# Kernel tuning notes

Measured on AMD Instinct MI355X. Metric: run time of the kernel, lower is better.

The kernel has to match this reference:

```python
import jax, jax.numpy as jnp
import numpy as np

V = 50257   # vocab / ouput_size
H = 1024    # hidden_size
L = 4096    # encoder length
NL = 2      # num_layers


def setup_inputs() -> dict:
    key = jax.random.key(0)
    ks = jax.random.split(key, 20)
    s = 0.02
    f32 = jnp.float32
    return {
        "input": jax.random.randint(ks[0], (1, 1), 0, V),
        "hidden_state": jax.random.normal(ks[1], (NL, 1, H), f32),
        "enc_outputs": jax.random.normal(ks[2], (L, H), f32),
        # parameters
        "emb": jax.random.normal(ks[3], (V, H), f32) * s,
        "Wq": jax.random.normal(ks[4], (H, H), f32) * s,
        "Wk": jax.random.normal(ks[5], (H, H), f32) * s,
        "wv": jax.random.normal(ks[6], (H, 1), f32) * s,
        "W_ih0": jax.random.normal(ks[7], (3 * H, 2 * H), f32) * s,
        "W_hh0": jax.random.normal(ks[8], (3 * H, H), f32) * s,
        "b_ih0": jnp.zeros((3 * H,), f32),
        "b_hh0": jnp.zeros((3 * H,), f32),
        "W_ih1": jax.random.normal(ks[9], (3 * H, H), f32) * s,
        "W_hh1": jax.random.normal(ks[10], (3 * H, H), f32) * s,
        "b_ih1": jnp.zeros((3 * H,), f32),
        "b_hh1": jnp.zeros((3 * H,), f32),
        "Wd": jax.random.normal(ks[11], (H, V), f32) * s,
        "bd": jnp.zeros((V,), f32),
    }


def _gru_step(x, h, W_ih, W_hh, b_ih, b_hh):
    # PyTorch GRU cell: gates ordered (reset, update, new)
    gi = W_ih @ x + b_ih          # [3H]
    gh = W_hh @ h + b_hh          # [3H]
    i_r, i_z, i_n = jnp.split(gi, 3)
    h_r, h_z, h_n = jnp.split(gh, 3)
    r = jax.nn.sigmoid(i_r + h_r)
    z = jax.nn.sigmoid(i_z + h_z)
    n = jnp.tanh(i_n + r * h_n)
    return (1.0 - z) * n + z * h


def reference(input, hidden_state, enc_outputs, emb, Wq, Wk, wv,
              W_ih0, W_hh0, b_ih0, b_hh0, W_ih1, W_hh1, b_ih1, b_hh1,
              Wd, bd):
    # embedding + (dropout p=0 is identity) + relu  -> [H]
    emb_vec = jax.nn.relu(emb[input[0, 0]])
    # additive attention: query = last-layer hidden [H], keys/values = enc [L,H]
    query = hidden_state[-1, 0]
    feat = jnp.tanh(query @ Wq + enc_outputs @ Wk)   # [L,H] (broadcast add)
    scores = feat @ wv                               # [L,1]
    attn = jax.nn.softmax(scores, axis=0)            # softmax over L
    context = jnp.sum(attn * enc_outputs, axis=0)    # [H]
    # single-step 2-layer GRU on concat(context, embedded) -> [2H]
    x = jnp.concatenate([context, emb_vec])
    h0n = _gru_step(x, hidden_state[0, 0], W_ih0, W_hh0, b_ih0, b_hh0)
    h1n = _gru_step(h0n, hidden_state[1, 0], W_ih1, W_hh1, b_ih1, b_hh1)
    # dense + log_softmax over vocab
    logits = h1n @ Wd + bd                           # [V]
    logp = jax.nn.log_softmax(logits)[None, :]       # [1,V]
    new_hidden = jnp.stack([h0n, h1n])[:, None, :]   # [NL,1,H]
    return logp, new_hidden
```

## Files before the change

### kernel.cpp

```cpp
#include <hip/hip_runtime.h>
#include <hip/hip_bf16.h>

#define H  1024
#define L  4096
#define V  50257
#define H3 3072

#define OFF_QW     0
#define OFF_SCORES 1024
#define OFF_X      (1024 + 4096)
#define OFF_GI0    (OFF_X + 2048)
#define OFF_GH0    (OFF_GI0 + 3072)
#define OFF_GI1    (OFF_GH0 + 3072)
#define OFF_GH1    (OFF_GI1 + 3072)
#define OFF_LOGITS (OFF_GH1 + 3072)
#define WS_FLOATS  (OFF_LOGITS + V)

__global__ __launch_bounds__(256) void k_embed(const int* __restrict__ tok,
                                               const float* __restrict__ emb,
                                               float* __restrict__ ws) {
    int j = blockIdx.x * 256 + threadIdx.x;
    int t = tok[0];
    float v = emb[(size_t)t * H + j];
    ws[OFF_X + H + j] = fmaxf(v, 0.f);
}

__global__ __launch_bounds__(256) void k_qw(const float* __restrict__ Wq,
                                            const float* __restrict__ hid,
                                            float* __restrict__ ws) {
    int j = blockIdx.x * 256 + threadIdx.x;
    const float* q = hid + H;
    int i0 = blockIdx.y * 64;
    float acc = 0.f;
#pragma unroll 8
    for (int i = i0; i < i0 + 64; ++i) acc += q[i] * Wq[i * H + j];
    atomicAdd(&ws[OFF_QW + j], acc);
}

__global__ __launch_bounds__(256) void k_gemm_scores(const float* __restrict__ enc,
                                                     const float* __restrict__ Wk,
                                                     const float* __restrict__ wv,
                                                     float* __restrict__ ws) {
    __shared__ float As[32][68];
    __shared__ float Bs[32][68];
    const int tid = threadIdx.x;
    const int tx = tid & 15, ty = tid >> 4;
    const int m0 = blockIdx.x * 64, n0 = blockIdx.y * 64;

    float acc[4][4] = {};

    for (int k0 = 0; k0 < H; k0 += 32) {
#pragma unroll
        for (int s = 0; s < 2; ++s) {
            int u  = tid + s * 256;
            int r  = u >> 3;
            int kq = u & 7;
            float4 a = *(const float4*)(enc + (m0 + r) * H + k0 + kq * 4);
            As[kq * 4 + 0][r] = a.x;
            As[kq * 4 + 1][r] = a.y;
            As[kq * 4 + 2][r] = a.z;
            As[kq * 4 + 3][r] = a.w;
        }
#pragma unroll
        for (int s = 0; s < 2; ++s) {
            int u  = tid + s * 256;
            int k  = u >> 4;
            int nq = u & 15;
            *(float4*)(&Bs[k][nq * 4]) = *(const float4*)(Wk + (k0 + k) * H + n0 + nq * 4);
        }
        __syncthreads();
#pragma unroll
        for (int k = 0; k < 32; ++k) {
            float4 a = *(const float4*)(&As[k][ty * 4]);
            float4 b = *(const float4*)(&Bs[k][tx * 4]);
            acc[0][0] += a.x * b.x; acc[0][1] += a.x * b.y; acc[0][2] += a.x * b.z; acc[0][3] += a.x * b.w;
            acc[1][0] += a.y * b.x; acc[1][1] += a.y * b.y; acc[1][2] += a.y * b.z; acc[1][3] += a.y * b.w;
            acc[2][0] += a.z * b.x; acc[2][1] += a.z * b.y; acc[2][2] += a.z * b.z; acc[2][3] += a.z * b.w;
            acc[3][0] += a.w * b.x; acc[3][1] += a.w * b.y; acc[3][2] += a.w * b.z; acc[3][3] += a.w * b.w;
        }
        __syncthreads();
    }

    float4 qw4 = *(const float4*)(&ws[OFF_QW + n0 + tx * 4]);
    float4 wv4 = *(const float4*)(wv + n0 + tx * 4);
#pragma unroll
    for (int i = 0; i < 4; ++i) {
        float s = tanhf(acc[i][0] + qw4.x) * wv4.x
                + tanhf(acc[i][1] + qw4.y) * wv4.y
                + tanhf(acc[i][2] + qw4.z) * wv4.z
                + tanhf(acc[i][3] + qw4.w) * wv4.w;
#pragma unroll
        for (int off = 1; off < 16; off <<= 1) s += __shfl_down(s, off, 16);
        if (tx == 0) atomicAdd(&ws[OFF_SCORES + m0 + ty * 4 + i], s);
    }
}

__global__ __launch_bounds__(1024) void k_softmax(float* __restrict__ ws) {
    __shared__ float red[16];
    const int tid = threadIdx.x;
    float* sc = ws + OFF_SCORES;

    float m = -1e30f;
    for (int l = tid; l < L; l += 1024) m = fmaxf(m, sc[l]);
#pragma unroll
    for (int off = 32; off; off >>= 1) m = fmaxf(m, __shfl_down(m, off));
    if ((tid & 63) == 0) red[tid >> 6] = m;
    __syncthreads();
    if (tid == 0) {
        float mm = red[0];
        for (int w = 1; w < 16; ++w) mm = fmaxf(mm, red[w]);
        red[0] = mm;
    }
    __syncthreads();
    m = red[0];
    __syncthreads();

    float ssum = 0.f;
    for (int l = tid; l < L; l += 1024) ssum += expf(sc[l] - m);
#pragma unroll
    for (int off = 32; off; off >>= 1) ssum += __shfl_down(ssum, off);
    if ((tid & 63) == 0) red[tid >> 6] = ssum;
    __syncthreads();
    if (tid == 0) {
        float t = 0.f;
        for (int w = 0; w < 16; ++w) t += red[w];
        red[0] = t;
    }
    __syncthreads();
    float inv = 1.f / red[0];

    for (int l = tid; l < L; l += 1024) sc[l] = expf(sc[l] - m) * inv;
}

__global__ __launch_bounds__(256) void k_context(const float* __restrict__ enc,
                                                 float* __restrict__ ws) {
    int h = blockIdx.x * 256 + threadIdx.x;
    const float* attn = ws + OFF_SCORES;
    int l0 = blockIdx.y * 128;
    float acc = 0.f;
#pragma unroll 4
    for (int l = l0; l < l0 + 128; ++l) acc += attn[l] * enc[l * H + h];
    atomicAdd(&ws[OFF_X + h], acc);
}

__global__ __launch_bounds__(256) void k_gates(const float* __restrict__ Wih,
                                               const float* __restrict__ Whh,
                                               const float* __restrict__ bih,
                                               const float* __restrict__ bhh,
                                               const float* __restrict__ x, int Cx,
                                               const float* __restrict__ h,
                                               float* __restrict__ gi,
                                               float* __restrict__ gh) {
    int b = blockIdx.x;
    bool isH = (b >= 768);
    int row  = (isH ? b - 768 : b) * 4 + (threadIdx.x >> 6);
    int lane = threadIdx.x & 63;
    const float* W    = isH ? Whh : Wih;
    const float* v    = isH ? h : x;
    const float* bias = isH ? bhh : bih;
    int C       = isH ? H : Cx;
    float* out  = isH ? gh : gi;

    const float4* Wr = (const float4*)(W + (size_t)row * C);
    const float4* v4 = (const float4*)v;
    float acc = 0.f;
    int n4 = C >> 2;
    for (int c = lane; c < n4; c += 64) {
        float4 w = Wr[c], xx = v4[c];
        acc += w.x * xx.x + w.y * xx.y + w.z * xx.z + w.w * xx.w;
    }
#pragma unroll
    for (int off = 32; off; off >>= 1) acc += __shfl_down(acc, off);
    if (lane == 0) out[row] = acc + bias[row];
}

__global__ __launch_bounds__(256) void k_combine(const float* __restrict__ gi,
                                                 const float* __restrict__ gh,
                                                 const float* __restrict__ h,
                                                 float* __restrict__ hout) {
    int j = blockIdx.x * 256 + threadIdx.x;
    float r = 1.f / (1.f + expf(-(gi[j] + gh[j])));
    float z = 1.f / (1.f + expf(-(gi[H + j] + gh[H + j])));
    float n = tanhf(gi[2 * H + j] + r * gh[2 * H + j]);
    hout[j] = (1.f - z) * n + z * h[j];
}

__global__ __launch_bounds__(256) void k_logits(const float* __restrict__ Wd,
                                                const float* __restrict__ bd,
                                                const float* __restrict__ h1,
                                                float* __restrict__ ws) {
    int v = blockIdx.x * 256 + threadIdx.x;
    if (v >= V) return;
    int k0 = blockIdx.y * 128;
    float acc = (blockIdx.y == 0) ? bd[v] : 0.f;
#pragma unroll 4
    for (int k = k0; k < k0 + 128; ++k) acc += h1[k] * Wd[(size_t)k * V + v];
    atomicAdd(&ws[OFF_LOGITS + v], acc);
}

__global__ __launch_bounds__(1024) void k_logsoftmax(const float* __restrict__ lg,
                                                     float* __restrict__ out) {
    __shared__ float red[16];
    const int tid = threadIdx.x;

    float m = -1e30f;
    for (int v = tid; v < V; v += 1024) m = fmaxf(m, lg[v]);
#pragma unroll
    for (int off = 32; off; off >>= 1) m = fmaxf(m, __shfl_down(m, off));
    if ((tid & 63) == 0) red[tid >> 6] = m;
    __syncthreads();
    if (tid == 0) {
        float mm = red[0];
        for (int w = 1; w < 16; ++w) mm = fmaxf(mm, red[w]);
        red[0] = mm;
    }
    __syncthreads();
    m = red[0];
    __syncthreads();

    float s = 0.f;
    for (int v = tid; v < V; v += 1024) s += expf(lg[v] - m);
#pragma unroll
    for (int off = 32; off; off >>= 1) s += __shfl_down(s, off);
    if ((tid & 63) == 0) red[tid >> 6] = s;
    __syncthreads();
    if (tid == 0) {
        float t = 0.f;
        for (int w = 0; w < 16; ++w) t += red[w];
        red[0] = t;
    }
    __syncthreads();
    float lse = m + logf(red[0]);

    for (int v = tid; v < V; v += 1024) out[v] = lg[v] - lse;
}

extern "C" void kernel_launch(void* const* d_in, const int* in_sizes, int n_in,
                              void* d_out, int out_size, void* d_ws, size_t ws_size,
                              hipStream_t stream) {
    const int*   tok  = (const int*)d_in[0];
    const float* hid  = (const float*)d_in[1];
    const float* enc  = (const float*)d_in[2];
    const float* emb  = (const float*)d_in[3];
    const float* Wq   = (const float*)d_in[4];
    const float* Wk   = (const float*)d_in[5];
    const float* wv   = (const float*)d_in[6];
    const float* Wih0 = (const float*)d_in[7];
    const float* Whh0 = (const float*)d_in[8];
    const float* bih0 = (const float*)d_in[9];
    const float* bhh0 = (const float*)d_in[10];
    const float* Wih1 = (const float*)d_in[11];
    const float* Whh1 = (const float*)d_in[12];
    const float* bih1 = (const float*)d_in[13];
    const float* bhh1 = (const float*)d_in[14];
    const float* Wd   = (const float*)d_in[15];
    const float* bd   = (const float*)d_in[16];
    float* out = (float*)d_out;
    float* ws  = (float*)d_ws;

    hipMemsetAsync(ws, 0, WS_FLOATS * sizeof(float), stream);

    k_embed<<<4, 256, 0, stream>>>(tok, emb, ws);
    k_qw<<<dim3(4, 16), 256, 0, stream>>>(Wq, hid, ws);
    k_gemm_scores<<<dim3(L / 64, H / 64), 256, 0, stream>>>(enc, Wk, wv, ws);
    k_softmax<<<1, 1024, 0, stream>>>(ws);
    k_context<<<dim3(4, 32), 256, 0, stream>>>(enc, ws);

    k_gates<<<1536, 256, 0, stream>>>(Wih0, Whh0, bih0, bhh0,
                                      ws + OFF_X, 2 * H, hid,
                                      ws + OFF_GI0, ws + OFF_GH0);
    k_combine<<<4, 256, 0, stream>>>(ws + OFF_GI0, ws + OFF_GH0, hid, out + V);

    k_gates<<<1536, 256, 0, stream>>>(Wih1, Whh1, bih1, bhh1,
                                      out + V, H, hid + H,
                                      ws + OFF_GI1, ws + OFF_GH1);
    k_combine<<<4, 256, 0, stream>>>(ws + OFF_GI1, ws + OFF_GH1, hid + H, out + V + H);

    k_logits<<<dim3((V + 255) / 256, 8), 256, 0, stream>>>(Wd, bd, out + V + H, ws);
    k_logsoftmax<<<1, 1024, 0, stream>>>(ws + OFF_LOGITS, out);
}
```

Measured before the change: 618.7 us.

## Use bf16 MFMA for attention scores GEMM and fuse softmax, GRU combine stages

Transposes Wk to bf16 in a combined prep kernel and computes the L×H attention-feature GEMM with 32x32x16 bf16 MFMA instructions instead of FP32 FMA tiling. The softmax is folded into the context kernel, and the GRU combine steps are folded into the next gates and logits kernels, which removes several launches. The cost is bf16 rounding of the encoder and Wk inputs, an extra transpose pass over Wk on every call, and redundant recomputation of the softmax statistics and GRU combine in every block.

```diff
diff --git a/kernel.cpp b/kernel.cpp
--- a/kernel.cpp
+++ b/kernel.cpp
@@ -4,143 +4,161 @@
 #define H  1024
 #define L  4096
 #define V  50257
-#define H3 3072
 
 #define OFF_QW     0
 #define OFF_SCORES 1024
-#define OFF_X      (1024 + 4096)
-#define OFF_GI0    (OFF_X + 2048)
-#define OFF_GH0    (OFF_GI0 + 3072)
-#define OFF_GI1    (OFF_GH0 + 3072)
-#define OFF_GH1    (OFF_GI1 + 3072)
-#define OFF_LOGITS (OFF_GH1 + 3072)
-#define WS_FLOATS  (OFF_LOGITS + V)
-
-__global__ __launch_bounds__(256) void k_embed(const int* __restrict__ tok,
-                                               const float* __restrict__ emb,
-                                               float* __restrict__ ws) {
-    int j = blockIdx.x * 256 + threadIdx.x;
-    int t = tok[0];
-    float v = emb[(size_t)t * H + j];
-    ws[OFF_X + H + j] = fmaxf(v, 0.f);
-}
-
-__global__ __launch_bounds__(256) void k_qw(const float* __restrict__ Wq,
-                                            const float* __restrict__ hid,
-                                            float* __restrict__ ws) {
-    int j = blockIdx.x * 256 + threadIdx.x;
-    const float* q = hid + H;
-    int i0 = blockIdx.y * 64;
-    float acc = 0.f;
+#define OFF_X      5120
+#define OFF_GI0    7168
+#define OFF_GH0    10240
+#define OFF_GI1    13312
+#define OFF_GH1    16384
+#define OFF_LOGITS 19456
+#define ZERO_FLOATS (OFF_LOGITS + V)
+#define OFF_WKT_BYTES 278880
+
+typedef __bf16 bf8   __attribute__((ext_vector_type(8)));
+typedef float  f32x16 __attribute__((ext_vector_type(16)));
+
+__device__ inline unsigned int pack_bf16x2(float lo, float hi) {
+    unsigned int ulo = __builtin_bit_cast(unsigned int, lo);
+    unsigned int uhi = __builtin_bit_cast(unsigned int, hi);
+    return ((uhi + 0x8000u) & 0xFFFF0000u) | ((ulo + 0x8000u) >> 16);
+}
+__device__ inline unsigned short cvt_bf16(float f) {
+    unsigned int u = __builtin_bit_cast(unsigned int, f);
+    return (unsigned short)((u + 0x8000u) >> 16);
+}
+
+__global__ __launch_bounds__(256) void k_prep(const int* __restrict__ tok,
+                                              const float* __restrict__ emb,
+                                              const float* __restrict__ hid,
+                                              const float* __restrict__ Wq,
+                                              const float* __restrict__ Wk,
+                                              float* __restrict__ ws,
+                                              unsigned short* __restrict__ wkT) {
+    __shared__ float tile[32][33];
+    const int b = blockIdx.x, t = threadIdx.x;
+    if (b < 4) {
+        int j = b * 256 + t;
+        float v = emb[(size_t)tok[0] * H + j];
+        ws[OFF_X + H + j] = fmaxf(v, 0.f);
+    } else if (b < 68) {
+        int bb = b - 4;
+        int j = (bb & 3) * 256 + t;
+        int i0 = (bb >> 2) * 64;
+        const float* q = hid + H;
+        float acc = 0.f;
 #pragma unroll 8
-    for (int i = i0; i < i0 + 64; ++i) acc += q[i] * Wq[i * H + j];
-    atomicAdd(&ws[OFF_QW + j], acc);
+        for (int i = i0; i < i0 + 64; ++i) acc += q[i] * Wq[i * H + j];
+        atomicAdd(&ws[OFF_QW + j], acc);
+    } else {
+        int tt = b - 68;
+        int tk = tt & 31, tn = tt >> 5;
+        int c = t & 31, r0 = t >> 5;
+#pragma unroll
+        for (int rr = 0; rr < 4; ++rr) {
+            int r = r0 + rr * 8;
+            tile[r][c] = Wk[(size_t)(tk * 32 + r) * H + tn * 32 + c];
+        }
+        __syncthreads();
+#pragma unroll
+        for (int rr = 0; rr < 4; ++rr) {
+            int rn = r0 + rr * 8;
+            wkT[(size_t)(tn * 32 + rn) * H + tk * 32 + c] = cvt_bf16(tile[c][rn]);
+        }
+    }
 }
 
 __global__ __launch_bounds__(256) void k_gemm_scores(const float* __restrict__ enc,
-                                                     const float* __restrict__ Wk,
+                                                     const unsigned short* __restrict__ wkT,
                                                      const float* __restrict__ wv,
                                                      float* __restrict__ ws) {
-    __shared__ float As[32][68];
-    __shared__ float Bs[32][68];
-    const int tid = threadIdx.x;
-    const int tx = tid & 15, ty = tid >> 4;
-    const int m0 = blockIdx.x * 64, n0 = blockIdx.y * 64;
-
-    float acc[4][4] = {};
+    __shared__ unsigned short As[64][40];
+    __shared__ unsigned short Bs[128][40];
+    const int t = threadIdx.x, lane = t & 63, w = t >> 6;
+    const int m0 = blockIdx.x * 64, n0 = blockIdx.y * 128;
+
+    f32x16 acc0 = {}, acc1 = {};
+
+    const int ar = t >> 2, akq = (t & 3) * 8;
+    const int bn = t >> 1, bkh = (t & 1) * 16;
+
+    const int r0 = (w & 1) * 32, c0 = (w >> 1) * 64;
+    const int mrow = r0 + (lane & 31);
+    const int nrow0 = c0 + (lane & 31), nrow1 = nrow0 + 32;
 
     for (int k0 = 0; k0 < H; k0 += 32) {
-#pragma unroll
-        for (int s = 0; s < 2; ++s) {
-            int u  = tid + s * 256;
-            int r  = u >> 3;
-            int kq = u & 7;
-            float4 a = *(const float4*)(enc + (m0 + r) * H + k0 + kq * 4);
-            As[kq * 4 + 0][r] = a.x;
-            As[kq * 4 + 1][r] = a.y;
-            As[kq * 4 + 2][r] = a.z;
-            As[kq * 4 + 3][r] = a.w;
-        }
-#pragma unroll
-        for (int s = 0; s < 2; ++s) {
-            int u  = tid + s * 256;
-            int k  = u >> 4;
-            int nq = u & 15;
-            *(float4*)(&Bs[k][nq * 4]) = *(const float4*)(Wk + (k0 + k) * H + n0 + nq * 4);
-        }
+        float4 fa = *(const float4*)(enc + (size_t)(m0 + ar) * H + k0 + akq);
+        float4 fb = *(const float4*)(enc + (size_t)(m0 + ar) * H + k0 + akq + 4);
+        uint4 wb0 = *(const uint4*)(wkT + (size_t)(n0 + bn) * H + k0 + bkh);
+        uint4 wb1 = *(const uint4*)(wkT + (size_t)(n0 + bn) * H + k0 + bkh + 8);
         __syncthreads();
-#pragma unroll
-        for (int k = 0; k < 32; ++k) {
-            float4 a = *(const float4*)(&As[k][ty * 4]);
-            float4 b = *(const float4*)(&Bs[k][tx * 4]);
-            acc[0][0] += a.x * b.x; acc[0][1] += a.x * b.y; acc[0][2] += a.x * b.z; acc[0][3] += a.x * b.w;
-            acc[1][0] += a.y * b.x; acc[1][1] += a.y * b.y; acc[1][2] += a.y * b.z; acc[1][3] += a.y * b.w;
-            acc[2][0] += a.z * b.x; acc[2][1] += a.z * b.y; acc[2][2] += a.z * b.z; acc[2][3] += a.z * b.w;
-            acc[3][0] += a.w * b.x; acc[3][1] += a.w * b.y; acc[3][2] += a.w * b.z; acc[3][3] += a.w * b.w;
-        }
+        uint4 pa;
+        pa.x = pack_bf16x2(fa.x, fa.y); pa.y = pack_bf16x2(fa.z, fa.w);
+        pa.z = pack_bf16x2(fb.x, fb.y); pa.w = pack_bf16x2(fb.z, fb.w);
+        *(uint4*)&As[ar][akq] = pa;
+        *(uint4*)&Bs[bn][bkh] = wb0;
+        *(uint4*)&Bs[bn][bkh + 8] = wb1;
         __syncthreads();
-    }
-
-    float4 qw4 = *(const float4*)(&ws[OFF_QW + n0 + tx * 4]);
-    float4 wv4 = *(const float4*)(wv + n0 + tx * 4);
-#pragma unroll
-    for (int i = 0; i < 4; ++i) {
-        float s = tanhf(acc[i][0] + qw4.x) * wv4.x
-                + tanhf(acc[i][1] + qw4.y) * wv4.y
-                + tanhf(acc[i][2] + qw4.z) * wv4.z
-                + tanhf(acc[i][3] + qw4.w) * wv4.w;
-#pragma unroll
-        for (int off = 1; off < 16; off <<= 1) s += __shfl_down(s, off, 16);
-        if (tx == 0) atomicAdd(&ws[OFF_SCORES + m0 + ty * 4 + i], s);
-    }
-}
-
-__global__ __launch_bounds__(1024) void k_softmax(float* __restrict__ ws) {
-    __shared__ float red[16];
-    const int tid = threadIdx.x;
-    float* sc = ws + OFF_SCORES;
-
-    float m = -1e30f;
-    for (int l = tid; l < L; l += 1024) m = fmaxf(m, sc[l]);
-#pragma unroll
-    for (int off = 32; off; off >>= 1) m = fmaxf(m, __shfl_down(m, off));
-    if ((tid & 63) == 0) red[tid >> 6] = m;
-    __syncthreads();
-    if (tid == 0) {
-        float mm = red[0];
-        for (int w = 1; w < 16; ++w) mm = fmaxf(mm, red[w]);
-        red[0] = mm;
-    }
-    __syncthreads();
-    m = red[0];
-    __syncthreads();
-
-    float ssum = 0.f;
-    for (int l = tid; l < L; l += 1024) ssum += expf(sc[l] - m);
-#pragma unroll
-    for (int off = 32; off; off >>= 1) ssum += __shfl_down(ssum, off);
-    if ((tid & 63) == 0) red[tid >> 6] = ssum;
-    __syncthreads();
-    if (tid == 0) {
-        float t = 0.f;
-        for (int w = 0; w < 16; ++w) t += red[w];
-        red[0] = t;
-    }
-    __syncthreads();
-    float inv = 1.f / red[0];
-
-    for (int l = tid; l < L; l += 1024) sc[l] = expf(sc[l] - m) * inv;
+#pragma unroll
+        for (int kk = 0; kk < 2; ++kk) {
+            int kb = kk * 16 + (lane >> 5) * 8;
+            bf8 a  = *(const bf8*)&As[mrow][kb];
+            bf8 b0 = *(const bf8*)&Bs[nrow0][kb];
+            bf8 b1 = *(const bf8*)&Bs[nrow1][kb];
+            acc0 = __builtin_amdgcn_mfma_f32_32x32x16_bf16(a, b0, acc0, 0, 0, 0);
+            acc1 = __builtin_amdgcn_mfma_f32_32x32x16_bf16(a, b1, acc1, 0, 0, 0);
+        }
+    }
+
+    const int n_a = n0 + nrow0, n_b = n0 + nrow1;
+    float qwa = ws[OFF_QW + n_a], qwb = ws[OFF_QW + n_b];
+    float wva = wv[n_a], wvb = wv[n_b];
+    const int rbase = m0 + r0 + 4 * (lane >> 5);
+#pragma unroll
+    for (int reg = 0; reg < 16; ++reg) {
+        float s = tanhf(acc0[reg] + qwa) * wva + tanhf(acc1[reg] + qwb) * wvb;
+#pragma unroll
+        for (int msk = 1; msk < 32; msk <<= 1) s += __shfl_xor(s, msk);
+        if ((lane & 31) == 0) {
+            int l = rbase + (reg & 3) + 8 * (reg >> 2);
+            atomicAdd(&ws[OFF_SCORES + l], s);
+        }
+    }
 }
 
 __global__ __launch_bounds__(256) void k_context(const float* __restrict__ enc,
                                                  float* __restrict__ ws) {
-    int h = blockIdx.x * 256 + threadIdx.x;
-    const float* attn = ws + OFF_SCORES;
-    int l0 = blockIdx.y * 128;
+    __shared__ float red[4];
+    const int t = threadIdx.x;
+    const float* sc = ws + OFF_SCORES;
+
+    float m = -1e30f;
+#pragma unroll
+    for (int i = 0; i < 16; ++i) m = fmaxf(m, sc[t + i * 256]);
+#pragma unroll
+    for (int msk = 1; msk < 64; msk <<= 1) m = fmaxf(m, __shfl_xor(m, msk));
+    if ((t & 63) == 0) red[t >> 6] = m;
+    __syncthreads();
+    m = fmaxf(fmaxf(red[0], red[1]), fmaxf(red[2], red[3]));
+    __syncthreads();
+
+    float s = 0.f;
+#pragma unroll
+    for (int i = 0; i < 16; ++i) s += expf(sc[t + i * 256] - m);
+#pragma unroll
+    for (int msk = 1; msk < 64; msk <<= 1) s += __shfl_xor(s, msk);
+    if ((t & 63) == 0) red[t >> 6] = s;
+    __syncthreads();
+    float inv = 1.f / (red[0] + red[1] + red[2] + red[3]);
+
+    const int h = blockIdx.x * 256 + t;
+    const int l0 = blockIdx.y * 128;
     float acc = 0.f;
 #pragma unroll 4
-    for (int l = l0; l < l0 + 128; ++l) acc += attn[l] * enc[l * H + h];
-    atomicAdd(&ws[OFF_X + h], acc);
+    for (int l = l0; l < l0 + 128; ++l)
+        acc += expf(sc[l] - m) * enc[(size_t)l * H + h];
+    atomicAdd(&ws[OFF_X + h], acc * inv);
 }
 
 __global__ __launch_bounds__(256) void k_gates(const float* __restrict__ Wih,
@@ -166,35 +184,92 @@
     float acc = 0.f;
     int n4 = C >> 2;
     for (int c = lane; c < n4; c += 64) {
-        float4 w = Wr[c], xx = v4[c];
-        acc += w.x * xx.x + w.y * xx.y + w.z * xx.z + w.w * xx.w;
+        float4 wv4 = Wr[c], xx = v4[c];
+        acc += wv4.x * xx.x + wv4.y * xx.y + wv4.z * xx.z + wv4.w * xx.w;
     }
 #pragma unroll
     for (int off = 32; off; off >>= 1) acc += __shfl_down(acc, off);
     if (lane == 0) out[row] = acc + bias[row];
 }
 
-__global__ __launch_bounds__(256) void k_combine(const float* __restrict__ gi,
-                                                 const float* __restrict__ gh,
-                                                 const float* __restrict__ h,
-                                                 float* __restrict__ hout) {
-    int j = blockIdx.x * 256 + threadIdx.x;
-    float r = 1.f / (1.f + expf(-(gi[j] + gh[j])));
-    float z = 1.f / (1.f + expf(-(gi[H + j] + gh[H + j])));
-    float n = tanhf(gi[2 * H + j] + r * gh[2 * H + j]);
-    hout[j] = (1.f - z) * n + z * h[j];
+__global__ __launch_bounds__(256) void k_gates1(const float* __restrict__ Wih,
+                                                const float* __restrict__ Whh,
+                                                const float* __restrict__ bih,
+                                                const float* __restrict__ bhh,
+                                                const float* __restrict__ gi0,
+                                                const float* __restrict__ gh0,
+                                                const float* __restrict__ hid,
+                                                float* __restrict__ h0n_out,
+                                                float* __restrict__ gi,
+                                                float* __restrict__ gh) {
+    const int b = blockIdx.x, t = threadIdx.x;
+    const int lane = t & 63;
+    if (b < 768) {
+        __shared__ float xs[H];
+#pragma unroll
+        for (int jj = 0; jj < 4; ++jj) {
+            int j = t + jj * 256;
+            float r = 1.f / (1.f + expf(-(gi0[j] + gh0[j])));
+            float z = 1.f / (1.f + expf(-(gi0[H + j] + gh0[H + j])));
+            float n = tanhf(gi0[2 * H + j] + r * gh0[2 * H + j]);
+            float h0 = (1.f - z) * n + z * hid[j];
+            xs[j] = h0;
+            if (b == 0) h0n_out[j] = h0;
+        }
+        __syncthreads();
+        int row = b * 4 + (t >> 6);
+        const float4* Wr = (const float4*)(Wih + (size_t)row * H);
+        float acc = 0.f;
+        for (int c = lane; c < H / 4; c += 64) {
+            float4 wv4 = Wr[c];
+            float4 xx = *(const float4*)&xs[c * 4];
+            acc += wv4.x * xx.x + wv4.y * xx.y + wv4.z * xx.z + wv4.w * xx.w;
+        }
+#pragma unroll
+        for (int off = 32; off; off >>= 1) acc += __shfl_down(acc, off);
+        if (lane == 0) gi[row] = acc + bih[row];
+    } else {
+        int row = (b - 768) * 4 + (t >> 6);
+        const float4* Wr = (const float4*)(Whh + (size_t)row * H);
+        const float4* h4 = (const float4*)(hid + H);
+        float acc = 0.f;
+        for (int c = lane; c < H / 4; c += 64) {
+            float4 wv4 = Wr[c], xx = h4[c];
+            acc += wv4.x * xx.x + wv4.y * xx.y + wv4.z * xx.z + wv4.w * xx.w;
+        }
+#pragma unroll
+        for (int off = 32; off; off >>= 1) acc += __shfl_down(acc, off);
+        if (lane == 0) gh[row] = acc + bhh[row];
+    }
 }
 
 __global__ __launch_bounds__(256) void k_logits(const float* __restrict__ Wd,
                                                 const float* __restrict__ bd,
-                                                const float* __restrict__ h1,
+                                                const float* __restrict__ gi1,
+                                                const float* __restrict__ gh1,
+                                                const float* __restrict__ hid,
+                                                float* __restrict__ h1n_out,
                                                 float* __restrict__ ws) {
-    int v = blockIdx.x * 256 + threadIdx.x;
+    __shared__ float h1s[H];
+    const int t = threadIdx.x;
+#pragma unroll
+    for (int jj = 0; jj < 4; ++jj) {
+        int j = t + jj * 256;
+        float r = 1.f / (1.f + expf(-(gi1[j] + gh1[j])));
+        float z = 1.f / (1.f + expf(-(gi1[H + j] + gh1[H + j])));
+        float n = tanhf(gi1[2 * H + j] + r * gh1[2 * H + j]);
+        float h1 = (1.f - z) * n + z * hid[H + j];
+        h1s[j] = h1;
+        if (blockIdx.x == 0 && blockIdx.y == 0) h1n_out[j] = h1;
+    }
+    __syncthreads();
+    int v = blockIdx.x * 256 + t;
     if (v >= V) return;
     int k0 = blockIdx.y * 128;
     float acc = (blockIdx.y == 0) ? bd[v] : 0.f;
-#pragma unroll 4
-    for (int k = k0; k < k0 + 128; ++k) acc += h1[k] * Wd[(size_t)k * V + v];
+    const float* Wp = Wd + (size_t)k0 * V + v;
+#pragma unroll 8
+    for (int k = 0; k < 128; ++k) acc += h1s[k0 + k] * Wp[(size_t)k * V];
     atomicAdd(&ws[OFF_LOGITS + v], acc);
 }
 
@@ -225,9 +300,9 @@
     if ((tid & 63) == 0) red[tid >> 6] = s;
     __syncthreads();
     if (tid == 0) {
-        float t = 0.f;
-        for (int w = 0; w < 16; ++w) t += red[w];
-        red[0] = t;
+        float tt = 0.f;
+        for (int w = 0; w < 16; ++w) tt += red[w];
+        red[0] = tt;
     }
     __syncthreads();
     float lse = m + logf(red[0]);
@@ -257,25 +332,21 @@
     const float* bd   = (const float*)d_in[16];
     float* out = (float*)d_out;
     float* ws  = (float*)d_ws;
-
-    hipMemsetAsync(ws, 0, WS_FLOATS * sizeof(float), stream);
-
-    k_embed<<<4, 256, 0, stream>>>(tok, emb, ws);
-    k_qw<<<dim3(4, 16), 256, 0, stream>>>(Wq, hid, ws);
-    k_gemm_scores<<<dim3(L / 64, H / 64), 256, 0, stream>>>(enc, Wk, wv, ws);
-    k_softmax<<<1, 1024, 0, stream>>>(ws);
+    unsigned short* wkT = (unsigned short*)((char*)d_ws + OFF_WKT_BYTES);
+
+    hipMemsetAsync(ws, 0, ZERO_FLOATS * sizeof(float), stream);
+
+    k_prep<<<1092, 256, 0, stream>>>(tok, emb, hid, Wq, Wk, ws, wkT);
+    k_gemm_scores<<<dim3(L / 64, H / 128), 256, 0, stream>>>(enc, wkT, wv, ws);
     k_context<<<dim3(4, 32), 256, 0, stream>>>(enc, ws);
-
     k_gates<<<1536, 256, 0, stream>>>(Wih0, Whh0, bih0, bhh0,
                                       ws + OFF_X, 2 * H, hid,
                                       ws + OFF_GI0, ws + OFF_GH0);
-    k_combine<<<4, 256, 0, stream>>>(ws + OFF_GI0, ws + OFF_GH0, hid, out + V);
-
-    k_gates<<<1536, 256, 0, stream>>>(Wih1, Whh1, bih1, bhh1,
-                                      out + V, H, hid + H,
-                                      ws + OFF_GI1, ws + OFF_GH1);
-    k_combine<<<4, 256, 0, stream>>>(ws + OFF_GI1, ws + OFF_GH1, hid + H, out + V + H);
-
-    k_logits<<<dim3((V + 255) / 256, 8), 256, 0, stream>>>(Wd, bd, out + V + H, ws);
+    k_gates1<<<1536, 256, 0, stream>>>(Wih1, Whh1, bih1, bhh1,
+                                       ws + OFF_GI0, ws + OFF_GH0, hid,
+                                       out + V, ws + OFF_GI1, ws + OFF_GH1);
+    k_logits<<<dim3((V + 255) / 256, 8), 256, 0, stream>>>(Wd, bd,
+                                       ws + OFF_GI1, ws + OFF_GH1, hid,
+                                       out + V + H, ws);
     k_logsoftmax<<<1, 1024, 0, stream>>>(ws + OFF_LOGITS, out);
 }
```

Result: faster. 530.8 us (-14.2%).
